# Kernel optimization log

Measured on AMD Instinct MI355X. Metric: run time of the kernel, lower is better.

Reference implementation:

```python
import jax, jax.numpy as jnp
import numpy as np

NUM_EMBEDDING = 8192
EMBEDDING_DIM = 512
BS = 16384
NEG_SLOPE = 0.01  # torch LeakyReLU default


def setup_inputs() -> dict:
    key = jax.random.key(0)
    k1, k2, k3, k4, k5, k6, k7 = jax.random.split(key, 7)
    d, K = EMBEDDING_DIM, NUM_EMBEDDING
    s1 = 1.0 / np.sqrt(d)
    return {
        "encoded_eeg": jax.random.normal(k1, (BS, d), dtype=jnp.float32),
        "encoded_mel": jax.random.normal(k2, (BS, d), dtype=jnp.float32),
        "embeddings": jax.random.normal(k3, (K, d), dtype=jnp.float32),
        "W1": jax.random.uniform(k4, (d, d), jnp.float32, -s1, s1),
        "b1": jax.random.uniform(k5, (d,), jnp.float32, -s1, s1),
        "W2": jax.random.uniform(k6, (K, d), jnp.float32, -s1, s1),
        "b2": jax.random.uniform(k7, (K,), jnp.float32, -s1, s1),
    }


def reference(encoded_eeg, encoded_mel, embeddings, W1, b1, W2, b2):
    # --- nearest-codebook indices for mel (detached in original) ---
    flat_mel = encoded_mel.reshape(-1, EMBEDDING_DIM)
    dists = (jnp.sum(embeddings ** 2, axis=1)[None, :]
             + jnp.sum(flat_mel ** 2, axis=1, keepdims=True)
             - 2.0 * flat_mel @ embeddings.T)  # [BS, K]
    mel_indices = jnp.argmin(dists, axis=-1)  # [BS]

    # --- small MLP logits over eeg ---
    flat_eeg = encoded_eeg.reshape(-1, EMBEDDING_DIM)
    h = flat_eeg @ W1.T + b1
    h = jnp.where(h >= 0, h, NEG_SLOPE * h)  # LeakyReLU
    logits = h @ W2.T + b2  # [BS, K]

    eeg_indices = jnp.argmax(logits, axis=-1)
    acc_rate = jnp.mean((eeg_indices == mel_indices).astype(jnp.float32))

    # cross entropy (mean over batch)
    logp = jax.nn.log_softmax(logits, axis=-1)
    loss = -jnp.mean(jnp.take_along_axis(logp, mel_indices[:, None], axis=1))
    return (loss, acc_rate)
```

## Files before the change

kernel.cpp:

```cpp
#include <hip/hip_runtime.h>
#include <hip/hip_bf16.h>
#include <hip/hip_fp8.h>

#define BSZ 16384
#define DIM 512
#define NEMB 8192
#define NEG 0.01f
#define NSPLIT 8

typedef __attribute__((ext_vector_type(8))) short short8;
typedef __attribute__((ext_vector_type(4))) float f32x4;
typedef __attribute__((ext_vector_type(4))) int i32x4;
typedef __attribute__((ext_vector_type(8))) int i32x8;

typedef const __attribute__((address_space(1))) void GVT;
typedef __attribute__((address_space(3))) void LVT;

__device__ __forceinline__ void gl_lds16(const void* g, void* l) {
    __builtin_amdgcn_global_load_lds((GVT*)g, (LVT*)l, 16, 0, 0);
}

__device__ __forceinline__ float bf2f(unsigned short u) {
    union { unsigned int i; float f; } c; c.i = ((unsigned int)u) << 16; return c.f;
}
__device__ __forceinline__ unsigned short f2bf(float f) {
    union { __hip_bfloat16 h; unsigned short u; } c; c.h = __float2bfloat16(f); return c.u;
}
__device__ __forceinline__ unsigned char f2fp8(float f) {
    __hip_fp8_e4m3 t(f); return (unsigned char)t.__x;
}
__device__ __forceinline__ unsigned int fkey(float f) {
    unsigned int u = __float_as_uint(f);
    return u ^ ((unsigned int)((int)u >> 31) | 0x80000000u);
}

__device__ __forceinline__ size_t pack_addr(int r, int k) {
    int kg = k >> 6, ko = k & 63;
    int half = ko >> 5, lq = (ko & 31) >> 3, sub = ko & 7;
    int L = lq * 16 + (r & 15);
    return ((size_t)((r >> 4) * 8 + kg) << 10) + (size_t)(L << 4) + (half << 3) + sub;
}

__device__ __forceinline__ void pipe_barrier8() {
    asm volatile("s_waitcnt vmcnt(8) lgkmcnt(0)\ns_barrier" ::: "memory");
}
__device__ __forceinline__ void drain_barrier() {
    asm volatile("s_waitcnt vmcnt(0) lgkmcnt(0)\ns_barrier" ::: "memory");
}
__device__ __forceinline__ void lgkm_barrier() {
    asm volatile("s_waitcnt lgkmcnt(0)\ns_barrier" ::: "memory");
}

#define ISSUE_NT(NT, BUF) do { \
    const unsigned char* src_ = gB0p + (size_t)(NT) * 32768; \
    _Pragma("unroll") for (int i_ = 0; i_ < 8; i_++) \
        gl_lds16(src_ + i_ * 1024, &sB8[BUF][uWd + i_ * 1024]); \
} while (0)

#define LOADH(VA, VB, CUR, HB, KP) do { \
    const unsigned char* lb_ = &sB8[CUR][((2 * (HB)) * 8 + 2 * (KP)) * 1024] + (lane << 4); \
    i32x4 a0_ = *(const i32x4*)lb_; \
    i32x4 a1_ = *(const i32x4*)(lb_ + 1024); \
    i32x4 b0_ = *(const i32x4*)(lb_ + 8192); \
    i32x4 b1_ = *(const i32x4*)(lb_ + 8192 + 1024); \
    VA = __builtin_shufflevector(a0_, a1_, 0, 1, 2, 3, 4, 5, 6, 7); \
    VB = __builtin_shufflevector(b0_, b1_, 0, 1, 2, 3, 4, 5, 6, 7); \
} while (0)

#define MFMA8(VA, VB, KP, FIRST) do { \
    __builtin_amdgcn_s_setprio(1); \
    _Pragma("unroll") for (int mi = 0; mi < 4; mi++) { \
        f32x4 c0_ = (FIRST) ? Z4 : acc[mi][0]; \
        f32x4 c1_ = (FIRST) ? Z4 : acc[mi][1]; \
        acc[mi][0] = __builtin_amdgcn_mfma_scale_f32_16x16x128_f8f6f4( \
            fa8[mi][KP], VA, c0_, 0, 0, 0, 0x7F7F7F7Fu, 0, 0x7F7F7F7Fu); \
        acc[mi][1] = __builtin_amdgcn_mfma_scale_f32_16x16x128_f8f6f4( \
            fa8[mi][KP], VB, c1_, 0, 0, 0, 0x7F7F7F7Fu, 0, 0x7F7F7F7Fu); \
    } \
    __builtin_amdgcn_s_setprio(0); \
} while (0)

#define EPI_HALF(NT, HB) do { \
    int j0 = ((NT) << 6) + ((HB) << 5) + l15; \
    if (is_logits) { \
        float bb0 = sAux[j0], bb1 = sAux[j0 + 16]; \
        unsigned int ic0 = (unsigned int)(NEMB - 1 - (nbase + j0)); \
        _Pragma("unroll") for (int mi = 0; mi < 4; mi++) \
            _Pragma("unroll") for (int rg = 0; rg < 4; rg++) { \
                float v0 = acc[mi][0][rg] + bb0; \
                float v1 = acc[mi][1][rg] + bb1; \
                int r = mi * 4 + rg; \
                s[r] += __expf(v0) + __expf(v1); \
                float m = fmaxf(v0, v1); \
                unsigned int ii = v1 > v0 ? ic0 - 16 : ic0; \
                unsigned int pk = (fkey(m) & 0xFFFFE000u) | ii; \
                pbest[r] = pbest[r] > pk ? pbest[r] : pk; \
            } \
    } else { \
        float en0 = sAux[j0], en1 = sAux[j0 + 16]; \
        unsigned int cl0 = (unsigned int)(nbase + j0); \
        _Pragma("unroll") for (int mi = 0; mi < 4; mi++) \
            _Pragma("unroll") for (int rg = 0; rg < 4; rg++) { \
                float v0 = fmaf(-2.f, acc[mi][0][rg], en0); \
                float v1 = fmaf(-2.f, acc[mi][1][rg], en1); \
                float m = fminf(v0, v1); \
                unsigned int ii = v1 < v0 ? cl0 + 16 : cl0; \
                unsigned int pk = (fkey(m) & 0xFFFFE000u) | ii; \
                int r = mi * 4 + rg; \
                pbest[r] = pbest[r] < pk ? pbest[r] : pk; \
            } \
    } \
} while (0)

#define HALF(NT, CUR, HB) do { \
    LOADH(fA0, fA1, CUR, HB, 0); \
    LOADH(fB0, fB1, CUR, HB, 1);  MFMA8(fA0, fA1, 0, 1); \
    LOADH(fA0, fA1, CUR, HB, 2);  MFMA8(fB0, fB1, 1, 0); \
    LOADH(fB0, fB1, CUR, HB, 3);  MFMA8(fA0, fA1, 2, 0); \
                                  MFMA8(fB0, fB1, 3, 0); \
    EPI_HALF(NT, HB); \
} while (0)

__global__ void k_prep(const float* __restrict__ eeg, const float* __restrict__ mel,
                       const float* __restrict__ emb, const float* __restrict__ W2,
                       const float* __restrict__ W1,
                       unsigned short* __restrict__ o_eeg, unsigned short* __restrict__ o_w1,
                       unsigned char* __restrict__ o_mel8, unsigned char* __restrict__ o_emb8,
                       unsigned char* __restrict__ o_w28,
                       float* __restrict__ enorm,
                       float* __restrict__ acc2, int* __restrict__ cnt) {
    int bid = blockIdx.x, tid = threadIdx.x;
    if (bid == 0 && tid == 0) { acc2[0] = 0.f; acc2[1] = 0.f; *cnt = 0; }
    if (bid < 1024) {
        const int n_big = BSZ * DIM / 4;
        const int n_mid = NEMB * DIM / 4;
        const int n_w1  = DIM * DIM / 4;
        const int total = n_big * 2 + n_mid * 2 + n_w1;
        for (int i = bid * 256 + tid; i < total; i += 1024 * 256) {
            int j = i;
            if (j < n_big) {
                float4 v = ((const float4*)eeg)[j];
                ushort4 o; o.x = f2bf(v.x); o.y = f2bf(v.y); o.z = f2bf(v.z); o.w = f2bf(v.w);
                ((ushort4*)o_eeg)[j] = o;
            } else if ((j -= n_big) < n_w1) {
                float4 v = ((const float4*)W1)[j];
                ushort4 o; o.x = f2bf(v.x); o.y = f2bf(v.y); o.z = f2bf(v.z); o.w = f2bf(v.w);
                ((ushort4*)o_w1)[j] = o;
            } else if ((j -= n_w1) < n_big) {
                float4 v = ((const float4*)mel)[j];
                uchar4 o; o.x = f2fp8(v.x); o.y = f2fp8(v.y); o.z = f2fp8(v.z); o.w = f2fp8(v.w);
                *(uchar4*)(o_mel8 + pack_addr(j >> 7, (j & 127) * 4)) = o;
            } else if ((j -= n_big) < n_mid) {
                float4 v = ((const float4*)emb)[j];
                uchar4 o; o.x = f2fp8(v.x); o.y = f2fp8(v.y); o.z = f2fp8(v.z); o.w = f2fp8(v.w);
                *(uchar4*)(o_emb8 + pack_addr(j >> 7, (j & 127) * 4)) = o;
            } else {
                j -= n_mid;
                float4 v = ((const float4*)W2)[j];
                uchar4 o; o.x = f2fp8(v.x); o.y = f2fp8(v.y); o.z = f2fp8(v.z); o.w = f2fp8(v.w);
                *(uchar4*)(o_w28 + pack_addr(j >> 7, (j & 127) * 4)) = o;
            }
        }
    } else {
        int w = tid >> 6, lane = tid & 63;
        int row0 = (bid - 1024) * 8 + w * 2;
        #pragma unroll
        for (int t = 0; t < 2; t++) {
            int row = row0 + t;
            const float4* p = (const float4*)(emb + (size_t)row * DIM) + lane * 2;
            float4 a = p[0], b = p[1];
            float s = a.x*a.x + a.y*a.y + a.z*a.z + a.w*a.w
                    + b.x*b.x + b.y*b.y + b.z*b.z + b.w*b.w;
            #pragma unroll
            for (int d = 1; d < 64; d <<= 1) s += __shfl_xor(s, d);
            if (lane == 0) enorm[row] = s;
        }
    }
}

__launch_bounds__(256, 2)
__global__ void k_hgemm(const unsigned short* __restrict__ A,
                        const unsigned short* __restrict__ B,
                        const float* __restrict__ b1,
                        unsigned short* __restrict__ H,
                        unsigned char* __restrict__ H8) {
    __shared__ __align__(16) unsigned short sA[4096], sB[4096];
    int tid = threadIdx.x;
    int w = tid >> 6, lane = tid & 63;
    int wr = w >> 1, wc = w & 1;
    int lquad = lane >> 4, l15 = lane & 15;
    int mt = blockIdx.x >> 2, nt = blockIdx.x & 3;
    int m0 = mt * 128, n0 = nt * 128;

    int e0 = w * 512 + lane * 8;
    int r0 = e0 >> 5, ce = e0 & 31;
    const unsigned short* gA0 = A + (m0 + r0) * DIM + ce;
    const unsigned short* gA1 = gA0 + 64 * DIM;
    const unsigned short* gB0 = B + (n0 + r0) * DIM + ce;
    const unsigned short* gB1 = gB0 + 64 * DIM;
    unsigned short* lA0 = sA + w * 512;  unsigned short* lA1 = sA + (w + 4) * 512;
    unsigned short* lB0 = sB + w * 512;  unsigned short* lB1 = sB + (w + 4) * 512;

    int offA[4], offB[4];
    #pragma unroll
    for (int i = 0; i < 4; i++) {
        offA[i] = (wr * 64 + i * 16 + l15) * 32 + lquad * 8;
        offB[i] = (wc * 64 + i * 16 + l15) * 32 + lquad * 8;
    }

    f32x4 acc[4][4];
    #pragma unroll
    for (int mi = 0; mi < 4; mi++)
        #pragma unroll
        for (int ni = 0; ni < 4; ni++) acc[mi][ni] = 0;

    for (int kk = 0; kk < 16; kk++) {
        gl_lds16(gA0, lA0); gl_lds16(gA1, lA1);
        gl_lds16(gB0, lB0); gl_lds16(gB1, lB1);
        gA0 += 32; gA1 += 32; gB0 += 32; gB1 += 32;
        __syncthreads();
        short8 af[4], bf_[4];
        #pragma unroll
        for (int i = 0; i < 4; i++) {
            af[i]  = *(const short8*)&sA[offA[i]];
            bf_[i] = *(const short8*)&sB[offB[i]];
        }
        #pragma unroll
        for (int mi = 0; mi < 4; mi++)
            #pragma unroll
            for (int ni = 0; ni < 4; ni++)
                acc[mi][ni] = __builtin_amdgcn_mfma_f32_16x16x32_bf16(af[mi], bf_[ni], acc[mi][ni], 0, 0, 0);
        __syncthreads();
    }

    #pragma unroll
    for (int ni = 0; ni < 4; ni++) {
        int col = n0 + wc * 64 + ni * 16 + l15;
        float bv = b1[col];
        #pragma unroll
        for (int mi = 0; mi < 4; mi++) {
            int rowb = m0 + wr * 64 + mi * 16 + lquad * 4;
            #pragma unroll
            for (int rg = 0; rg < 4; rg++) {
                float v = acc[mi][ni][rg] + bv;
                v = v >= 0.f ? v : NEG * v;
                H[(rowb + rg) * DIM + col] = f2bf(v);
                H8[pack_addr(rowb + rg, col)] = f2fp8(v);
            }
        }
    }
}

__launch_bounds__(256, 2)
__global__ void k_big(const unsigned char* __restrict__ Mel8,
                      const unsigned char* __restrict__ Emb8,
                      const unsigned char* __restrict__ H8,
                      const unsigned char* __restrict__ W28,
                      const float* __restrict__ enorm,
                      const float* __restrict__ b2,
                      float* __restrict__ p_s,
                      unsigned int* __restrict__ p_pmax,
                      unsigned int* __restrict__ p_pmin) {
    __shared__ __align__(16) unsigned char sB8[2][32768];
    __shared__ float sAux[1024];
    int tid = threadIdx.x;
    int w = tid >> 6, lane = tid & 63;
    int lquad = lane >> 4, l15 = lane & 15;
    int bid = blockIdx.x;
    int split = bid & 7;
    int is_logits = (bid >> 3) & 1;
    int mt = bid >> 4;
    int m0 = mt * 256, nbase = split * (NEMB / NSPLIT);

    const unsigned char* gAb = (is_logits ? H8 : Mel8);
    const unsigned char* gBb = (is_logits ? W28 : Emb8);

    #pragma unroll
    for (int j = 0; j < 4; j++) {
        int c = tid + j * 256;
        sAux[c] = is_logits ? b2[nbase + c] : (enorm[nbase + c] - 512.0f);
    }

    i32x8 fa8[4][4];
    #pragma unroll
    for (int mi = 0; mi < 4; mi++)
        #pragma unroll
        for (int kp = 0; kp < 4; kp++) {
            const unsigned char* p = gAb
                + ((size_t)(((m0 >> 4) + 4 * w + mi) * 8 + 2 * kp) << 10) + lane * 16;
            i32x4 lo = *(const i32x4*)p;
            i32x4 hi = *(const i32x4*)(p + 1024);
            fa8[mi][kp] = __builtin_shufflevector(lo, hi, 0, 1, 2, 3, 4, 5, 6, 7);
        }
    __syncthreads();

    int uWd = w * 8192;
    const unsigned char* gB0p = gBb + (size_t)nbase * 512 + uWd + lane * 16;

    const f32x4 Z4 = {0.f, 0.f, 0.f, 0.f};
    f32x4 acc[4][2];
    i32x8 fA0, fA1, fB0, fB1;

    float s[16];
    unsigned int pbest[16];
    unsigned int pinit = is_logits ? 0u : 0xFFFFFFFFu;
    #pragma unroll
    for (int r = 0; r < 16; r++) { s[r] = 0.f; pbest[r] = pinit; }

    ISSUE_NT(0, 0);
    for (int nt = 0; nt < 16; nt++) {
        int cur = nt & 1;
        if (nt < 15) { ISSUE_NT(nt + 1, cur ^ 1); pipe_barrier8(); }
        else         { drain_barrier(); }
        HALF(nt, cur, 0);
        HALF(nt, cur, 1);
        lgkm_barrier();
    }

    if (is_logits) {
        #pragma unroll
        for (int r = 0; r < 16; r++)
            #pragma unroll
            for (int d = 1; d < 16; d <<= 1) {
                s[r] += __shfl_xor(s[r], d);
                unsigned int o = (unsigned int)__shfl_xor((int)pbest[r], d);
                pbest[r] = pbest[r] > o ? pbest[r] : o;
            }
        if (l15 == 0) {
            #pragma unroll
            for (int mi = 0; mi < 4; mi++)
                #pragma unroll
                for (int rg = 0; rg < 4; rg++) {
                    int row = w * 64 + mi * 16 + lquad * 4 + rg;
                    int pidx = split * BSZ + m0 + row;
                    p_s[pidx] = s[mi * 4 + rg];
                    p_pmax[pidx] = pbest[mi * 4 + rg];
                }
        }
    } else {
        #pragma unroll
        for (int r = 0; r < 16; r++)
            #pragma unroll
            for (int d = 1; d < 16; d <<= 1) {
                unsigned int o = (unsigned int)__shfl_xor((int)pbest[r], d);
                pbest[r] = pbest[r] < o ? pbest[r] : o;
            }
        if (l15 == 0) {
            #pragma unroll
            for (int mi = 0; mi < 4; mi++)
                #pragma unroll
                for (int rg = 0; rg < 4; rg++) {
                    int row = w * 64 + mi * 16 + lquad * 4 + rg;
                    p_pmin[split * BSZ + m0 + row] = pbest[mi * 4 + rg];
                }
        }
    }
}

__global__ void k_tail(const float* __restrict__ p_s, const unsigned int* __restrict__ p_pmax,
                       const unsigned int* __restrict__ p_pmin,
                       const unsigned short* __restrict__ H,
                       const float* __restrict__ W2,
                       const float* __restrict__ b2,
                       float* __restrict__ acc2, int* __restrict__ cnt,
                       float* __restrict__ out) {
    __shared__ int s_idx[256];
    __shared__ float s_l1[256], s_match[256];
    __shared__ float s_d[4];
    int bid = blockIdx.x, tid = threadIdx.x;
    int w = tid >> 6, lane = tid & 63;
    int r = bid * 256 + tid;

    float S = 0.f; unsigned int PM = 0u, PN = 0xFFFFFFFFu;
    #pragma unroll
    for (int sp = 0; sp < NSPLIT; sp++) {
        S += p_s[sp * BSZ + r];
        unsigned int a = p_pmax[sp * BSZ + r];
        PM = PM > a ? PM : a;
        unsigned int b = p_pmin[sp * BSZ + r];
        PN = PN < b ? PN : b;
    }
    int eidx = (NEMB - 1) - (int)(PM & 0x1FFFu);
    int midx = (int)(PN & 0x1FFFu);
    s_idx[tid] = midx;
    s_l1[tid] = __logf(S) - b2[midx];
    s_match[tid] = (eidx == midx) ? 1.f : 0.f;
    __syncthreads();

    float d0 = 0.f, d1 = 0.f;
    for (int j = 0; j < 64; j++) {
        int rr = w * 64 + j;
        int ridx = s_idx[rr];
        uint4 hv = *(const uint4*)(H + (size_t)(bid * 256 + rr) * DIM + lane * 8);
        const float4* wp = (const float4*)(W2 + (size_t)ridx * DIM + lane * 8);
        float4 w0 = wp[0], w1 = wp[1];
        float p = bf2f((unsigned short)(hv.x & 0xffff)) * w0.x + bf2f((unsigned short)(hv.x >> 16)) * w0.y
                + bf2f((unsigned short)(hv.y & 0xffff)) * w0.z + bf2f((unsigned short)(hv.y >> 16)) * w0.w
                + bf2f((unsigned short)(hv.z & 0xffff)) * w1.x + bf2f((unsigned short)(hv.z >> 16)) * w1.y
                + bf2f((unsigned short)(hv.w & 0xffff)) * w1.z + bf2f((unsigned short)(hv.w >> 16)) * w1.w;
        if (j & 1) d1 += p; else d0 += p;
    }
    float ds = d0 + d1;
    #pragma unroll
    for (int d = 1; d < 64; d <<= 1) ds += __shfl_xor(ds, d);
    if (lane == 0) s_d[w] = ds;

    __syncthreads();
    for (int st = 128; st > 0; st >>= 1) {
        if (tid < st) { s_l1[tid] += s_l1[tid + st]; s_match[tid] += s_match[tid + st]; }
        __syncthreads();
    }
    if (tid == 0) {
        float loss_blk = s_l1[0] - (s_d[0] + s_d[1] + s_d[2] + s_d[3]);
        atomicAdd(&acc2[0], loss_blk * (1.0f / BSZ));
        atomicAdd(&acc2[1], s_match[0] * (1.0f / BSZ));
        __threadfence();
        if (atomicAdd(cnt, 1) == 63) {
            float L = atomicAdd(&acc2[0], 0.f);
            float M = atomicAdd(&acc2[1], 0.f);
            out[0] = L; out[1] = M;
        }
    }
}

extern "C" void kernel_launch(void* const* d_in, const int* in_sizes, int n_in,
                              void* d_out, int out_size, void* d_ws, size_t ws_size,
                              hipStream_t stream) {
    const float* eeg = (const float*)d_in[0];
    const float* mel = (const float*)d_in[1];
    const float* emb = (const float*)d_in[2];
    const float* W1  = (const float*)d_in[3];
    const float* b1  = (const float*)d_in[4];
    const float* W2  = (const float*)d_in[5];
    const float* b2  = (const float*)d_in[6];
    float* out = (float*)d_out;

    unsigned short* ws_eeg = (unsigned short*)d_ws;
    unsigned short* ws_w1  = ws_eeg + (size_t)BSZ * DIM;
    unsigned short* ws_h   = ws_w1  + (size_t)DIM * DIM;
    unsigned char*  ws_h8  = (unsigned char*)(ws_h + (size_t)BSZ * DIM);
    unsigned char*  ws_mel8 = ws_h8  + (size_t)BSZ * DIM;
    unsigned char*  ws_emb8 = ws_mel8 + (size_t)BSZ * DIM;
    unsigned char*  ws_w28  = ws_emb8 + (size_t)NEMB * DIM;
    float* ws_en  = (float*)(ws_w28 + (size_t)NEMB * DIM);
    float* p_s    = ws_en + NEMB;
    unsigned int* p_pmax = (unsigned int*)(p_s + (size_t)NSPLIT * BSZ);
    unsigned int* p_pmin = p_pmax + (size_t)NSPLIT * BSZ;
    float* acc2   = (float*)(p_pmin + (size_t)NSPLIT * BSZ);
    int*   cnt    = (int*)(acc2 + 2);

    k_prep<<<2048, 256, 0, stream>>>(eeg, mel, emb, W2, W1,
                                     ws_eeg, ws_w1, ws_mel8, ws_emb8, ws_w28,
                                     ws_en, acc2, cnt);
    k_hgemm<<<(BSZ / 128) * (DIM / 128), 256, 0, stream>>>(ws_eeg, ws_w1, b1, ws_h, ws_h8);
    k_big<<<(BSZ / 256) * NSPLIT * 2, 256, 0, stream>>>(ws_mel8, ws_emb8, ws_h8, ws_w28,
                                                        ws_en, b2, p_s, p_pmax, p_pmin);
    k_tail<<<BSZ / 256, 256, 0, stream>>>(p_s, p_pmax, p_pmin, ws_h, W2, b2, acc2, cnt, out);
}
```

Before: 359.8 us.

## Halve k_big M-tile and B-tile, raise occupancy, prefetch two tiles ahead

```diff
diff --git a/kernel.cpp b/kernel.cpp
--- a/kernel.cpp
+++ b/kernel.cpp
@@ -41,10 +41,10 @@
     return ((size_t)((r >> 4) * 8 + kg) << 10) + (size_t)(L << 4) + (half << 3) + sub;
 }
 
-__device__ __forceinline__ void pipe_barrier8() {
-    asm volatile("s_waitcnt vmcnt(8) lgkmcnt(0)\ns_barrier" ::: "memory");
-}
-__device__ __forceinline__ void drain_barrier() {
+__device__ __forceinline__ void vm4_barrier() {
+    asm volatile("s_waitcnt vmcnt(4) lgkmcnt(0)\ns_barrier" ::: "memory");
+}
+__device__ __forceinline__ void vm0_barrier() {
     asm volatile("s_waitcnt vmcnt(0) lgkmcnt(0)\ns_barrier" ::: "memory");
 }
 __device__ __forceinline__ void lgkm_barrier() {
@@ -52,40 +52,47 @@
 }
 
 #define ISSUE_NT(NT, BUF) do { \
-    const unsigned char* src_ = gB0p + (size_t)(NT) * 32768; \
-    _Pragma("unroll") for (int i_ = 0; i_ < 8; i_++) \
+    const unsigned char* src_ = gB0p + (size_t)(NT) * 16384; \
+    _Pragma("unroll") for (int i_ = 0; i_ < 4; i_++) \
         gl_lds16(src_ + i_ * 1024, &sB8[BUF][uWd + i_ * 1024]); \
 } while (0)
 
-#define LOADH(VA, VB, CUR, HB, KP) do { \
-    const unsigned char* lb_ = &sB8[CUR][((2 * (HB)) * 8 + 2 * (KP)) * 1024] + (lane << 4); \
+#define LOADH(F0, F1, CUR, KP) do { \
+    const unsigned char* lb_ = &sB8[CUR][(2 * (KP)) * 1024] + (lane << 4); \
     i32x4 a0_ = *(const i32x4*)lb_; \
     i32x4 a1_ = *(const i32x4*)(lb_ + 1024); \
     i32x4 b0_ = *(const i32x4*)(lb_ + 8192); \
     i32x4 b1_ = *(const i32x4*)(lb_ + 8192 + 1024); \
-    VA = __builtin_shufflevector(a0_, a1_, 0, 1, 2, 3, 4, 5, 6, 7); \
-    VB = __builtin_shufflevector(b0_, b1_, 0, 1, 2, 3, 4, 5, 6, 7); \
+    F0 = __builtin_shufflevector(a0_, a1_, 0, 1, 2, 3, 4, 5, 6, 7); \
+    F1 = __builtin_shufflevector(b0_, b1_, 0, 1, 2, 3, 4, 5, 6, 7); \
 } while (0)
 
-#define MFMA8(VA, VB, KP, FIRST) do { \
+#define MFMA4(F0, F1, KP, FIRST) do { \
     __builtin_amdgcn_s_setprio(1); \
-    _Pragma("unroll") for (int mi = 0; mi < 4; mi++) { \
+    _Pragma("unroll") for (int mi = 0; mi < 2; mi++) { \
         f32x4 c0_ = (FIRST) ? Z4 : acc[mi][0]; \
         f32x4 c1_ = (FIRST) ? Z4 : acc[mi][1]; \
         acc[mi][0] = __builtin_amdgcn_mfma_scale_f32_16x16x128_f8f6f4( \
-            fa8[mi][KP], VA, c0_, 0, 0, 0, 0x7F7F7F7Fu, 0, 0x7F7F7F7Fu); \
+            fa8[mi][KP], F0, c0_, 0, 0, 0, 0x7F7F7F7Fu, 0, 0x7F7F7F7Fu); \
         acc[mi][1] = __builtin_amdgcn_mfma_scale_f32_16x16x128_f8f6f4( \
-            fa8[mi][KP], VB, c1_, 0, 0, 0, 0x7F7F7F7Fu, 0, 0x7F7F7F7Fu); \
+            fa8[mi][KP], F1, c1_, 0, 0, 0, 0x7F7F7F7Fu, 0, 0x7F7F7F7Fu); \
     } \
     __builtin_amdgcn_s_setprio(0); \
 } while (0)
 
-#define EPI_HALF(NT, HB) do { \
-    int j0 = ((NT) << 6) + ((HB) << 5) + l15; \
+#define COMPUTE(CUR) do { \
+    LOADH(fB0, fB1, CUR, 0);  MFMA4(fB0, fB1, 0, 1); \
+    LOADH(fB0, fB1, CUR, 1);  MFMA4(fB0, fB1, 1, 0); \
+    LOADH(fB0, fB1, CUR, 2);  MFMA4(fB0, fB1, 2, 0); \
+    LOADH(fB0, fB1, CUR, 3);  MFMA4(fB0, fB1, 3, 0); \
+} while (0)
+
+#define EPILOGUE(NT) do { \
+    int j0 = ((NT) << 5) + l15; \
     if (is_logits) { \
         float bb0 = sAux[j0], bb1 = sAux[j0 + 16]; \
         unsigned int ic0 = (unsigned int)(NEMB - 1 - (nbase + j0)); \
-        _Pragma("unroll") for (int mi = 0; mi < 4; mi++) \
+        _Pragma("unroll") for (int mi = 0; mi < 2; mi++) \
             _Pragma("unroll") for (int rg = 0; rg < 4; rg++) { \
                 float v0 = acc[mi][0][rg] + bb0; \
                 float v1 = acc[mi][1][rg] + bb1; \
@@ -99,7 +106,7 @@
     } else { \
         float en0 = sAux[j0], en1 = sAux[j0 + 16]; \
         unsigned int cl0 = (unsigned int)(nbase + j0); \
-        _Pragma("unroll") for (int mi = 0; mi < 4; mi++) \
+        _Pragma("unroll") for (int mi = 0; mi < 2; mi++) \
             _Pragma("unroll") for (int rg = 0; rg < 4; rg++) { \
                 float v0 = fmaf(-2.f, acc[mi][0][rg], en0); \
                 float v1 = fmaf(-2.f, acc[mi][1][rg], en1); \
@@ -110,15 +117,6 @@
                 pbest[r] = pbest[r] < pk ? pbest[r] : pk; \
             } \
     } \
-} while (0)
-
-#define HALF(NT, CUR, HB) do { \
-    LOADH(fA0, fA1, CUR, HB, 0); \
-    LOADH(fB0, fB1, CUR, HB, 1);  MFMA8(fA0, fA1, 0, 1); \
-    LOADH(fA0, fA1, CUR, HB, 2);  MFMA8(fB0, fB1, 1, 0); \
-    LOADH(fB0, fB1, CUR, HB, 3);  MFMA8(fA0, fA1, 2, 0); \
-                                  MFMA8(fB0, fB1, 3, 0); \
-    EPI_HALF(NT, HB); \
 } while (0)
 
 __global__ void k_prep(const float* __restrict__ eeg, const float* __restrict__ mel,
@@ -251,7 +249,7 @@
     }
 }
 
-__launch_bounds__(256, 2)
+__launch_bounds__(256, 4)
 __global__ void k_big(const unsigned char* __restrict__ Mel8,
                       const unsigned char* __restrict__ Emb8,
                       const unsigned char* __restrict__ H8,
@@ -261,7 +259,7 @@
                       float* __restrict__ p_s,
                       unsigned int* __restrict__ p_pmax,
                       unsigned int* __restrict__ p_pmin) {
-    __shared__ __align__(16) unsigned char sB8[2][32768];
+    __shared__ __align__(16) unsigned char sB8[2][16384];
     __shared__ float sAux[1024];
     int tid = threadIdx.x;
     int w = tid >> 6, lane = tid & 63;
@@ -270,7 +268,7 @@
     int split = bid & 7;
     int is_logits = (bid >> 3) & 1;
     int mt = bid >> 4;
-    int m0 = mt * 256, nbase = split * (NEMB / NSPLIT);
+    int m0 = mt * 128, nbase = split * (NEMB / NSPLIT);
 
     const unsigned char* gAb = (is_logits ? H8 : Mel8);
     const unsigned char* gBb = (is_logits ? W28 : Emb8);
@@ -281,45 +279,47 @@
         sAux[c] = is_logits ? b2[nbase + c] : (enorm[nbase + c] - 512.0f);
     }
 
-    i32x8 fa8[4][4];
-    #pragma unroll
-    for (int mi = 0; mi < 4; mi++)
+    i32x8 fa8[2][4];
+    #pragma unroll
+    for (int mi = 0; mi < 2; mi++)
         #pragma unroll
         for (int kp = 0; kp < 4; kp++) {
             const unsigned char* p = gAb
-                + ((size_t)(((m0 >> 4) + 4 * w + mi) * 8 + 2 * kp) << 10) + lane * 16;
+                + ((size_t)(((m0 >> 4) + 2 * w + mi) * 8 + 2 * kp) << 10) + lane * 16;
             i32x4 lo = *(const i32x4*)p;
             i32x4 hi = *(const i32x4*)(p + 1024);
             fa8[mi][kp] = __builtin_shufflevector(lo, hi, 0, 1, 2, 3, 4, 5, 6, 7);
         }
+
+    int uWd = w * 4096;
+    const unsigned char* gB0p = gBb + (size_t)nbase * 512 + uWd + lane * 16;
+
     __syncthreads();
 
-    int uWd = w * 8192;
-    const unsigned char* gB0p = gBb + (size_t)nbase * 512 + uWd + lane * 16;
-
     const f32x4 Z4 = {0.f, 0.f, 0.f, 0.f};
-    f32x4 acc[4][2];
-    i32x8 fA0, fA1, fB0, fB1;
-
-    float s[16];
-    unsigned int pbest[16];
+    f32x4 acc[2][2];
+    i32x8 fB0, fB1;
+
+    float s[8];
+    unsigned int pbest[8];
     unsigned int pinit = is_logits ? 0u : 0xFFFFFFFFu;
     #pragma unroll
-    for (int r = 0; r < 16; r++) { s[r] = 0.f; pbest[r] = pinit; }
+    for (int r = 0; r < 8; r++) { s[r] = 0.f; pbest[r] = pinit; }
 
     ISSUE_NT(0, 0);
-    for (int nt = 0; nt < 16; nt++) {
+    ISSUE_NT(1, 1);
+    for (int nt = 0; nt < 32; nt++) {
         int cur = nt & 1;
-        if (nt < 15) { ISSUE_NT(nt + 1, cur ^ 1); pipe_barrier8(); }
-        else         { drain_barrier(); }
-        HALF(nt, cur, 0);
-        HALF(nt, cur, 1);
+        if (nt < 31) vm4_barrier(); else vm0_barrier();
+        COMPUTE(cur);
         lgkm_barrier();
+        if (nt + 2 < 32) ISSUE_NT(nt + 2, cur);
+        EPILOGUE(nt);
     }
 
     if (is_logits) {
         #pragma unroll
-        for (int r = 0; r < 16; r++)
+        for (int r = 0; r < 8; r++)
             #pragma unroll
             for (int d = 1; d < 16; d <<= 1) {
                 s[r] += __shfl_xor(s[r], d);
@@ -328,10 +328,10 @@
             }
         if (l15 == 0) {
             #pragma unroll
-            for (int mi = 0; mi < 4; mi++)
+            for (int mi = 0; mi < 2; mi++)
                 #pragma unroll
                 for (int rg = 0; rg < 4; rg++) {
-                    int row = w * 64 + mi * 16 + lquad * 4 + rg;
+                    int row = w * 32 + mi * 16 + lquad * 4 + rg;
                     int pidx = split * BSZ + m0 + row;
                     p_s[pidx] = s[mi * 4 + rg];
                     p_pmax[pidx] = pbest[mi * 4 + rg];
@@ -339,7 +339,7 @@
         }
     } else {
         #pragma unroll
-        for (int r = 0; r < 16; r++)
+        for (int r = 0; r < 8; r++)
             #pragma unroll
             for (int d = 1; d < 16; d <<= 1) {
                 unsigned int o = (unsigned int)__shfl_xor((int)pbest[r], d);
@@ -347,10 +347,10 @@
             }
         if (l15 == 0) {
             #pragma unroll
-            for (int mi = 0; mi < 4; mi++)
+            for (int mi = 0; mi < 2; mi++)
                 #pragma unroll
                 for (int rg = 0; rg < 4; rg++) {
-                    int row = w * 64 + mi * 16 + lquad * 4 + rg;
+                    int row = w * 32 + mi * 16 + lquad * 4 + rg;
                     p_pmin[split * BSZ + m0 + row] = pbest[mi * 4 + rg];
                 }
         }
@@ -453,7 +453,7 @@
                                      ws_eeg, ws_w1, ws_mel8, ws_emb8, ws_w28,
                                      ws_en, acc2, cnt);
     k_hgemm<<<(BSZ / 128) * (DIM / 128), 256, 0, stream>>>(ws_eeg, ws_w1, b1, ws_h, ws_h8);
-    k_big<<<(BSZ / 256) * NSPLIT * 2, 256, 0, stream>>>(ws_mel8, ws_emb8, ws_h8, ws_w28,
+    k_big<<<(BSZ / 128) * NSPLIT * 2, 256, 0, stream>>>(ws_mel8, ws_emb8, ws_h8, ws_w28,
                                                         ws_en, b2, p_s, p_pmax, p_pmin);
     k_tail<<<BSZ / 256, 256, 0, stream>>>(p_s, p_pmax, p_pmin, ws_h, W2, b2, acc2, cnt, out);
 }
```

Result: slower. 412.9 us (+14.8%).
